# Kernel optimization log

Hardware: AMD Instinct MI355X
Metric: run time of the kernel (lower is better)

The kernel has to match this reference:

```python
import jax, jax.numpy as jnp
import numpy as np

SB_EPSILON = 0.1
SB_SIZE = 1

B, S, L = 16, 256, 24


def _shift(x, axis, k):
    """y[..., i, ...] = x[..., i + k, ...], zero-padded out of range."""
    if k == 0:
        return x
    n = x.shape[axis]
    if k > 0:
        body = jax.lax.slice_in_dim(x, k, n, axis=axis)
        pad = jnp.zeros_like(jax.lax.slice_in_dim(x, 0, k, axis=axis))
        return jnp.concatenate([body, pad], axis=axis)
    k = -k
    body = jax.lax.slice_in_dim(x, 0, n - k, axis=axis)
    pad = jnp.zeros_like(jax.lax.slice_in_dim(x, 0, k, axis=axis))
    return jnp.concatenate([pad, body], axis=axis)


def setup_inputs() -> dict:
    key = jax.random.key(0)
    k1, k2 = jax.random.split(key)
    predict = jax.random.normal(k1, (B, S, S, L), dtype=jnp.float32)
    target = (jax.random.uniform(k2, (B, S, S, L)) < 0.002).astype(jnp.float32)
    # valid spans: end >= start
    tri = (jnp.arange(S)[None, :] >= jnp.arange(S)[:, None]).astype(jnp.int32)
    mask = jnp.broadcast_to(tri[None, :, :, None], (B, S, S, L)).astype(jnp.int32)
    # keep targets only on valid spans
    target = target * mask.astype(jnp.float32)
    return {"predict": predict, "target": target, "mask": mask}


def reference(predict, target, mask):
    dt = predict.dtype
    P = (target == 1).astype(dt)            # positive spans [B,S,S,L]
    M = (mask == 1).astype(dt)              # valid-span mask
    # subtract full epsilon from each positive span
    b2l = jnp.where(target == 1, target - SB_EPSILON, target)
    for dist in range(1, SB_SIZE + 1):
        eps = SB_EPSILON / (SB_SIZE * dist * 4)
        cnt = jnp.zeros_like(P)   # num valid neighbors per positive span
        add = jnp.zeros_like(P)   # smoothing mass scattered onto neighbors
        # NOTE: original code offsets neighbors by sb_size (not dist); identical for sb_size=1
        for axis, k in ((2, SB_SIZE), (2, -SB_SIZE), (1, SB_SIZE), (1, -SB_SIZE)):
            cnt = cnt + _shift(M, axis, k)          # neighbor in range and mask==1
            add = add + _shift(P, axis, -k)         # positives scattering into this cell
        b2l = b2l + eps * (add * M + P * (dist * 4 - cnt))
    # masked BCE-with-logits, mean over mask==1 elements
    x, t = predict, b2l
    bce = jnp.maximum(x, 0) - x * t + jnp.log1p(jnp.exp(-jnp.abs(x)))
    denom = jnp.sum(M)
    return jnp.sum(bce * M) / denom
```

## Files before the change

### kernel.cpp

```cpp
#include <hip/hip_runtime.h>


#define SS 256
#define LL 24

typedef float    fvec4 __attribute__((ext_vector_type(4)));
typedef unsigned uvec4 __attribute__((ext_vector_type(4)));

constexpr float EPS4      = 0.025f;
constexpr float INV_DENOM = 1.0f / 12632064.0f;
constexpr int   NT        = 256;
constexpr int   NB        = 16 * 128;
constexpr int   TOTAL6    = 257 * 6;
constexpr float LOG2E     = 1.4426950408889634f;
constexpr float LN2       = 0.6931471805599453f;

__device__ __forceinline__ float sp_part(float x) {
    float u = __builtin_amdgcn_exp2f(-LOG2E * fabsf(x));
    return fmaxf(x, 0.f) + LN2 * __builtin_amdgcn_logf(1.f + u);
}

__device__ __forceinline__ void process(const fvec4& x, const uvec4& t,
                                        int v, int q, int lenA6, int iA, int iB,
                                        const float* __restrict__ predf,
                                        float& acc, float& corr) {
    acc += sp_part(x.x) + sp_part(x.y) + sp_part(x.z) + sp_part(x.w);

    if ((t.x | t.y | t.z | t.w) != 0u) {
        bool inA = v < lenA6;
        int  vloc = inA ? v : (v - lenA6);
        int  i    = inA ? iA : iB;
        int  j    = i + vloc / 6;
        bool hasL = j > i;
        bool hasR = j < SS - 1;
        bool hasU = i > 0;
        float cnt = (hasL ? 2.f : 0.f) + (hasR ? 1.f : 0.f) + (hasU ? 1.f : 0.f);
        int ebase = q * 4;
        unsigned tu[4] = {t.x, t.y, t.z, t.w};
        float    xv[4] = {x.x, x.y, x.z, x.w};
#pragma unroll
        for (int k = 0; k < 4; ++k) {
            if (tu[k] != 0u) {
                int e = ebase + k;
                float s = 0.f;
                if (hasL) s += predf[e - LL];
                if (hasR) s += predf[e + LL];
                if (hasU) s += predf[e - LL * SS];
                if (hasL) s += predf[e + LL * SS];
                corr += fmaf(EPS4, s - xv[k] * cnt, xv[k]);
            }
        }
    }
}

__global__ __launch_bounds__(NT) void bs_pair(const fvec4* __restrict__ pred4,
                                              const uvec4* __restrict__ targ4,
                                              const float* __restrict__ predf,
                                              float* __restrict__ partial) {
    const int b  = blockIdx.x >> 7;
    const int iA = blockIdx.x & 127;
    const int iB = 255 - iA;
    const int lenA6 = (SS - iA) * 6;
    const int qA  = (((b << 8) + iA) * SS + iA) * 6;
    const int qB  = (((b << 8) + iB) * SS + iB) * 6;
    const int qB2 = qB - lenA6;

    float acc  = 0.f;
    float corr = 0.f;

    int v0 = threadIdx.x;
    int q0 = ((v0 < lenA6) ? qA : qB2) + v0;
    fvec4 x0 = __builtin_nontemporal_load(pred4 + q0);
    uvec4 t0 = __builtin_nontemporal_load(targ4 + q0);

    int  v1 = v0 + NT;
    bool m1 = v1 < TOTAL6;
    int q1 = 0; fvec4 x1; uvec4 t1;
    if (m1) {
        q1 = ((v1 < lenA6) ? qA : qB2) + v1;
        x1 = __builtin_nontemporal_load(pred4 + q1);
        t1 = __builtin_nontemporal_load(targ4 + q1);
    }

    for (;;) {
        int  v2 = v0 + 2 * NT;
        bool m2 = v2 < TOTAL6;
        int q2 = 0; fvec4 x2; uvec4 t2;
        if (m2) {
            q2 = ((v2 < lenA6) ? qA : qB2) + v2;
            x2 = __builtin_nontemporal_load(pred4 + q2);
            t2 = __builtin_nontemporal_load(targ4 + q2);
        }

        process(x0, t0, v0, q0, lenA6, iA, iB, predf, acc, corr);

        if (!m1) break;
        v0 = v1; q0 = q1; x0 = x1; t0 = t1;
        v1 = v2; q1 = q2; x1 = x2; t1 = t2;
        m1 = m2;
    }

    float vsum = acc - corr;

#pragma unroll
    for (int off = 32; off; off >>= 1) vsum += __shfl_down(vsum, off, 64);
    __shared__ float s[NT / 64];
    int w = threadIdx.x >> 6;
    if ((threadIdx.x & 63) == 0) s[w] = vsum;
    __syncthreads();
    if (threadIdx.x == 0) {
        float bsum = 0.f;
#pragma unroll
        for (int k = 0; k < NT / 64; ++k) bsum += s[k];
        partial[blockIdx.x] = bsum;
    }
}

__global__ __launch_bounds__(256) void bs_final(const float* __restrict__ partial,
                                                float* __restrict__ out) {
    float acc = 0.f;
#pragma unroll
    for (int k = threadIdx.x; k < NB; k += 256) acc += partial[k];
#pragma unroll
    for (int off = 32; off; off >>= 1) acc += __shfl_down(acc, off, 64);
    __shared__ float s[4];
    int w = threadIdx.x >> 6;
    if ((threadIdx.x & 63) == 0) s[w] = acc;
    __syncthreads();
    if (threadIdx.x == 0)
        out[0] = (s[0] + s[1] + s[2] + s[3]) * INV_DENOM;
}

extern "C" void kernel_launch(void* const* d_in, const int* in_sizes, int n_in,
                              void* d_out, int out_size, void* d_ws, size_t ws_size,
                              hipStream_t stream) {
    const fvec4* pred4 = (const fvec4*)d_in[0];
    const uvec4* targ4 = (const uvec4*)d_in[1];
    const float* predf = (const float*)d_in[0];
    float* partial = (float*)d_ws;
    float* out     = (float*)d_out;

    bs_pair <<<NB, NT, 0, stream>>>(pred4, targ4, predf, partial);
    bs_final<<<1, 256, 0, stream>>>(partial, out);
}
```

Measured before the change: 232.9 us.

## Flatten upper-triangle work into grid-stride loop with per-element index decode

Replaces the paired-row block assignment (row i with row 255-i per block) with a flat grid-stride enumeration over all valid upper-triangle vec4 elements. Each element's (batch, i, j) is recovered by integer division plus a sqrt-based triangular inverse with correction steps. This is meant to give perfectly uniform work per thread and smoother, more contiguous access across the grid. In exchange it adds per-element divide and sqrt arithmetic, and each thread's consecutive elements are now a full grid stride apart rather than adjacent within one block's rows.

```diff
diff --git a/kernel.cpp b/kernel.cpp
--- a/kernel.cpp
+++ b/kernel.cpp
@@ -7,13 +7,34 @@
 typedef float    fvec4 __attribute__((ext_vector_type(4)));
 typedef unsigned uvec4 __attribute__((ext_vector_type(4)));
 
-constexpr float EPS4      = 0.025f;
-constexpr float INV_DENOM = 1.0f / 12632064.0f;
-constexpr int   NT        = 256;
-constexpr int   NB        = 16 * 128;
-constexpr int   TOTAL6    = 257 * 6;
-constexpr float LOG2E     = 1.4426950408889634f;
-constexpr float LN2       = 0.6931471805599453f;
+constexpr float    EPS4      = 0.025f;
+constexpr float    INV_DENOM = 1.0f / 12632064.0f;
+constexpr int      NT        = 256;
+constexpr int      NB        = 2048;
+constexpr unsigned PERB6     = 197376u;
+constexpr unsigned TOT6      = 16u * PERB6;
+constexpr unsigned STRIDE    = (unsigned)(NB * NT);
+constexpr float    LOG2E     = 1.4426950408889634f;
+constexpr float    LN2       = 0.6931471805599453f;
+
+__device__ __forceinline__ int tri_prefix(int i) {
+    return (i * (513 - i)) >> 1;
+}
+
+__device__ __forceinline__ int decode_q(unsigned u, int& i_out, int& j_out) {
+    unsigned b = u / PERB6;
+    unsigned r = u - b * PERB6;
+    unsigned c = r / 6u;
+    unsigned m = r - c * 6u;
+    float disc = (float)(263169u - 8u * c);
+    int i = (int)((513.0f - sqrtf(disc)) * 0.5f);
+    if (tri_prefix(i) > (int)c) --i;
+    if (tri_prefix(i + 1) <= (int)c) ++i;
+    int j = i + ((int)c - tri_prefix(i));
+    i_out = i;
+    j_out = j;
+    return (int)(((b << 8) + (unsigned)i) * 256u + (unsigned)j) * 6 + (int)m;
+}
 
 __device__ __forceinline__ float sp_part(float x) {
     float u = __builtin_amdgcn_exp2f(-LOG2E * fabsf(x));
@@ -21,16 +42,12 @@
 }
 
 __device__ __forceinline__ void process(const fvec4& x, const uvec4& t,
-                                        int v, int q, int lenA6, int iA, int iB,
+                                        int i, int j, int q,
                                         const float* __restrict__ predf,
                                         float& acc, float& corr) {
     acc += sp_part(x.x) + sp_part(x.y) + sp_part(x.z) + sp_part(x.w);
 
     if ((t.x | t.y | t.z | t.w) != 0u) {
-        bool inA = v < lenA6;
-        int  vloc = inA ? v : (v - lenA6);
-        int  i    = inA ? iA : iB;
-        int  j    = i + vloc / 6;
         bool hasL = j > i;
         bool hasR = j < SS - 1;
         bool hasU = i > 0;
@@ -53,50 +70,43 @@
     }
 }
 
-__global__ __launch_bounds__(NT) void bs_pair(const fvec4* __restrict__ pred4,
+__global__ __launch_bounds__(NT) void bs_flat(const fvec4* __restrict__ pred4,
                                               const uvec4* __restrict__ targ4,
                                               const float* __restrict__ predf,
                                               float* __restrict__ partial) {
-    const int b  = blockIdx.x >> 7;
-    const int iA = blockIdx.x & 127;
-    const int iB = 255 - iA;
-    const int lenA6 = (SS - iA) * 6;
-    const int qA  = (((b << 8) + iA) * SS + iA) * 6;
-    const int qB  = (((b << 8) + iB) * SS + iB) * 6;
-    const int qB2 = qB - lenA6;
-
     float acc  = 0.f;
     float corr = 0.f;
 
-    int v0 = threadIdx.x;
-    int q0 = ((v0 < lenA6) ? qA : qB2) + v0;
+    unsigned u0 = blockIdx.x * NT + threadIdx.x;
+    int i0, j0;
+    int q0 = decode_q(u0, i0, j0);
     fvec4 x0 = __builtin_nontemporal_load(pred4 + q0);
     uvec4 t0 = __builtin_nontemporal_load(targ4 + q0);
 
-    int  v1 = v0 + NT;
-    bool m1 = v1 < TOTAL6;
-    int q1 = 0; fvec4 x1; uvec4 t1;
+    unsigned u1 = u0 + STRIDE;
+    bool m1 = u1 < TOT6;
+    int i1 = 0, j1 = 0, q1 = 0; fvec4 x1; uvec4 t1;
     if (m1) {
-        q1 = ((v1 < lenA6) ? qA : qB2) + v1;
+        q1 = decode_q(u1, i1, j1);
         x1 = __builtin_nontemporal_load(pred4 + q1);
         t1 = __builtin_nontemporal_load(targ4 + q1);
     }
 
     for (;;) {
-        int  v2 = v0 + 2 * NT;
-        bool m2 = v2 < TOTAL6;
-        int q2 = 0; fvec4 x2; uvec4 t2;
+        unsigned u2 = u0 + 2 * STRIDE;
+        bool m2 = u2 < TOT6;
+        int i2 = 0, j2 = 0, q2 = 0; fvec4 x2; uvec4 t2;
         if (m2) {
-            q2 = ((v2 < lenA6) ? qA : qB2) + v2;
+            q2 = decode_q(u2, i2, j2);
             x2 = __builtin_nontemporal_load(pred4 + q2);
             t2 = __builtin_nontemporal_load(targ4 + q2);
         }
 
-        process(x0, t0, v0, q0, lenA6, iA, iB, predf, acc, corr);
+        process(x0, t0, i0, j0, q0, predf, acc, corr);
 
         if (!m1) break;
-        v0 = v1; q0 = q1; x0 = x1; t0 = t1;
-        v1 = v2; q1 = q2; x1 = x2; t1 = t2;
+        u0 = u1; q0 = q1; i0 = i1; j0 = j1; x0 = x1; t0 = t1;
+        u1 = u2; q1 = q2; i1 = i2; j1 = j2; x1 = x2; t1 = t2;
         m1 = m2;
     }
 
@@ -140,6 +150,6 @@
     float* partial = (float*)d_ws;
     float* out     = (float*)d_out;
 
-    bs_pair <<<NB, NT, 0, stream>>>(pred4, targ4, predf, partial);
+    bs_flat <<<NB, NT, 0, stream>>>(pred4, targ4, predf, partial);
     bs_final<<<1, 256, 0, stream>>>(partial, out);
 }
```

Result: no change. 234.8 us (+0.8%).
